# Kernel tuning notes

Measured on AMD Instinct MI355X. Metric: run time of the kernel, lower is better.

The kernel has to match this reference:

```python
import jax, jax.numpy as jnp
import numpy as np

B, H, W, C = 32, 512, 512, 3


def dct2_matrix(N):
    # Orthonormal DCT-II basis: D[k, n] = s_k * sqrt(2/N) * cos(pi*(2n+1)*k/(2N))
    n = np.arange(N)
    k = n[:, None]
    D = np.cos(np.pi * (2 * n[None, :] + 1) * k / (2.0 * N)) * np.sqrt(2.0 / N)
    D[0, :] *= 1.0 / np.sqrt(2.0)  # ortho scaling of DC row
    return jnp.asarray(D, dtype=jnp.float32)


def setup_inputs() -> dict:
    key = jax.random.key(0)
    x = jax.random.normal(key, (B, H, W, C), dtype=jnp.float32)
    return {"x": x}


def reference(x) -> jnp.ndarray:
    # 2D DCT-II (ortho) along height and width, channels untouched.
    Dh = dct2_matrix(x.shape[1])  # [H, H]
    Dw = dct2_matrix(x.shape[2])  # [W, W]
    y = jnp.einsum('kh,bhwc->bkwc', Dh, x)   # DCT over height
    y = jnp.einsum('lw,bkwc->bklc', Dw, y)   # DCT over width
    return y
```

## Files before the change

### kernel.cpp

```cpp
#include <hip/hip_runtime.h>
#include <stdint.h>


typedef __bf16 bf16_t;
typedef bf16_t bf16x8 __attribute__((ext_vector_type(8)));
typedef float  f32x4  __attribute__((ext_vector_type(4)));

__device__ __forceinline__ uint32_t f2bf(float f) {
    union { float f; uint32_t u; } v; v.f = f;
    uint32_t r = v.u + 0x7fffu + ((v.u >> 16) & 1u);
    return r >> 16;
}

__device__ __forceinline__ f32x4 mfma16(bf16x8 a, bf16x8 b, f32x4 c) {
    return __builtin_amdgcn_mfma_f32_16x16x32_bf16(a, b, c, 0, 0, 0);
}

__device__ __forceinline__ void load_lds16(const void* g, void* l) {
    __builtin_amdgcn_global_load_lds(
        (const __attribute__((address_space(1))) uint32_t*)g,
        (__attribute__((address_space(3))) uint32_t*)l, 16, 0, 0);
}

__global__ __launch_bounds__(256) void gen_dct(uint16_t* __restrict__ Dbf) {
    int idx = blockIdx.x * 256 + threadIdx.x;
    int k = idx >> 9, h = idx & 511;
    int phase = ((2 * h + 1) * k) & 2047;
    float ang = (float)phase * 3.0679615757712823e-3f;
    float s = (k == 0) ? 0.04419417382415922f : 0.0625f;
    Dbf[idx] = (uint16_t)f2bf(__cosf(ang) * s);
}

__global__ __launch_bounds__(256) void xpose(const float* __restrict__ x,
                                             uint16_t* __restrict__ Xt) {
    const int jt = blockIdx.x, hb = blockIdx.y, b = blockIdx.z;
    const int t = threadIdx.x;
    const int jl = t & 127, hh = t >> 7;
    const int jg = jt * 128 + jl;
    const int w = jg / 3, c = jg - 3 * w;
    const int wr = ((w >> 8) << 8) + ((w & 255) >> 1) + ((w & 1) << 7);
    const int jr = c * 512 + wr;
    const float* src = x + (size_t)b * 786432 +
                       (size_t)(hb * 32 + hh * 16) * 1536 + jg;
    float v[16];
#pragma unroll
    for (int r = 0; r < 16; ++r) v[r] = src[(size_t)r * 1536];
    uint32_t p[8];
#pragma unroll
    for (int i = 0; i < 8; ++i)
        p[i] = f2bf(v[2 * i]) | (f2bf(v[2 * i + 1]) << 16);
    size_t dst = ((size_t)b * 1536 + jr) * 512 + hb * 32 + hh * 16;
    *(uint4*)&Xt[dst]     = make_uint4(p[0], p[1], p[2], p[3]);
    *(uint4*)&Xt[dst + 8] = make_uint4(p[4], p[5], p[6], p[7]);
}

__global__ __launch_bounds__(512, 2) void gemm1(const uint16_t* __restrict__ Xt,
                                                const uint16_t* __restrict__ Dbf,
                                                uint16_t* __restrict__ Y) {
    __shared__ __align__(16) uint16_t Al[128 * 64];
    __shared__ __align__(16) uint16_t Bl[256 * 64];
    const int t = threadIdx.x;
    const int lane = t & 63, wv = t >> 6;
    const int wm = wv >> 2, wn = wv & 3;
    const int nt = blockIdx.x;
    const int mt = blockIdx.y;
    const int b  = blockIdx.z;

    const int qa0 = t, qa1 = t + 512;
    const int ma0 = qa0 >> 3, ga0 = (qa0 & 7) ^ (ma0 & 7);
    const int ma1 = qa1 >> 3, ga1 = (qa1 & 7) ^ (ma1 & 7);
    const uint16_t* As0 = Dbf + (size_t)(mt * 128 + ma0) * 512 + ga0 * 8;
    const uint16_t* As1 = Dbf + (size_t)(mt * 128 + ma1) * 512 + ga1 * 8;
    const uint16_t* Bs[4];
    int qb[4];
#pragma unroll
    for (int i = 0; i < 4; ++i) {
        qb[i] = t + 512 * i;
        int mb = qb[i] >> 3, gb = (qb[i] & 7) ^ (mb & 7);
        Bs[i] = Xt + ((size_t)b * 1536 + nt * 256 + mb) * 512 + gb * 8;
    }

    f32x4 acc[4][4] = {};

    for (int kt = 0; kt < 8; ++kt) {
        __syncthreads();
        load_lds16(As0 + kt * 64, Al + qa0 * 8);
        load_lds16(As1 + kt * 64, Al + qa1 * 8);
#pragma unroll
        for (int i = 0; i < 4; ++i)
            load_lds16(Bs[i] + kt * 64, Bl + qb[i] * 8);
        __syncthreads();

#pragma unroll
        for (int ks = 0; ks < 2; ++ks) {
            bf16x8 aq[4], bq[4];
#pragma unroll
            for (int mf = 0; mf < 4; ++mf) {
                int row = wm * 64 + mf * 16 + (lane & 15);
                int sl = (ks * 4 + (lane >> 4)) ^ (row & 7);
                aq[mf] = *(const bf16x8*)&Al[row * 64 + sl * 8];
            }
#pragma unroll
            for (int f = 0; f < 4; ++f) {
                int col = (wn + 4 * f) * 16 + (lane & 15);
                int sl = (ks * 4 + (lane >> 4)) ^ (col & 7);
                bq[f] = *(const bf16x8*)&Bl[col * 64 + sl * 8];
            }
#pragma unroll
            for (int mf = 0; mf < 4; ++mf)
#pragma unroll
                for (int f = 0; f < 4; ++f)
                    acc[mf][f] = mfma16(aq[mf], bq[f], acc[mf][f]);
        }
    }

    const int cch = nt >> 1, whalf = nt & 1;
#pragma unroll
    for (int mf = 0; mf < 4; ++mf)
#pragma unroll
        for (int fp = 0; fp < 2; ++fp) {
            int kbase = mt * 128 + wm * 64 + mf * 16 + ((lane >> 4) << 2);
            int u = wn + 4 * fp;
            int w = whalf * 256 + 2 * (u * 16 + (lane & 15));
#pragma unroll
            for (int r = 0; r < 4; ++r) {
                uint32_t pk = f2bf(acc[mf][fp][r]) |
                              (f2bf(acc[mf][fp + 2][r]) << 16);
                *(uint32_t*)&Y[(size_t)b * 786432 + (size_t)(kbase + r) * 1536 +
                               cch * 512 + w] = pk;
            }
        }
}

__global__ __launch_bounds__(512, 4) void gemm2(const uint16_t* __restrict__ Y,
                                                const uint16_t* __restrict__ Dbf,
                                                float* __restrict__ out) {
    __shared__ __align__(16) char smem[49408];
    uint16_t* Al = (uint16_t*)smem;
    uint16_t* Bl = (uint16_t*)(smem + 12288);
    float*    El = (float*)smem;
    const int t = threadIdx.x;
    const int lane = t & 63, wv = t >> 6;
    const int wm = wv >> 2, wn = wv & 3;
    const int mt = blockIdx.x;
    const int lt = blockIdx.y;
    const int b  = blockIdx.z;
    const size_t yb = (size_t)b * 786432;

    const int qa0 = t, qa1 = t + 512;
    const int ma0 = qa0 >> 3, ga0 = (qa0 & 7) ^ (ma0 & 7);
    const int ma1 = qa1 >> 3, ga1 = (qa1 & 7) ^ (ma1 & 7);
    const uint16_t* As0 = Y + yb + (size_t)(mt * 96 + ma0) * 512 + ga0 * 8;
    const uint16_t* As1 = Y + yb + (size_t)(mt * 96 + ma1) * 512 + ga1 * 8;
    const uint16_t* Bs[4];
    int qb[4];
#pragma unroll
    for (int i = 0; i < 4; ++i) {
        qb[i] = t + 512 * i;
        int mb = qb[i] >> 3, gb = (qb[i] & 7) ^ (mb & 7);
        Bs[i] = Dbf + (size_t)(lt * 256 + mb) * 512 + gb * 8;
    }

    f32x4 acc[3][4] = {};

    for (int kt = 0; kt < 8; ++kt) {
        __syncthreads();
        load_lds16(As0 + kt * 64, Al + qa0 * 8);
        if (t < 256) load_lds16(As1 + kt * 64, Al + qa1 * 8);
#pragma unroll
        for (int i = 0; i < 4; ++i)
            load_lds16(Bs[i] + kt * 64, Bl + qb[i] * 8);
        __syncthreads();

#pragma unroll
        for (int ks = 0; ks < 2; ++ks) {
            bf16x8 aq[3], bq[4];
#pragma unroll
            for (int mf = 0; mf < 3; ++mf) {
                int row = wm * 48 + mf * 16 + (lane & 15);
                int sl = (ks * 4 + (lane >> 4)) ^ (row & 7);
                aq[mf] = *(const bf16x8*)&Al[row * 64 + sl * 8];
            }
#pragma unroll
            for (int f = 0; f < 4; ++f) {
                int col = wn * 64 + f * 16 + (lane & 15);
                int sl = (ks * 4 + (lane >> 4)) ^ (col & 7);
                bq[f] = *(const bf16x8*)&Bl[col * 64 + sl * 8];
            }
#pragma unroll
            for (int mf = 0; mf < 3; ++mf)
#pragma unroll
                for (int f = 0; f < 4; ++f)
                    acc[mf][f] = mfma16(aq[mf], bq[f], acc[mf][f]);
        }
    }

    const int kloc = t >> 5, zrow = t & 31;
#pragma unroll
    for (int rnd = 0; rnd < 2; ++rnd) {
        __syncthreads();
        if (wm == rnd) {
#pragma unroll
            for (int mf = 0; mf < 3; ++mf)
#pragma unroll
                for (int f = 0; f < 4; ++f) {
                    int row = mf * 16 + ((lane >> 4) << 2);
                    int col = wn * 64 + f * 16 + (lane & 15);
#pragma unroll
                    for (int r = 0; r < 4; ++r)
                        El[(row + r) * 257 + col] = acc[mf][f][r];
                }
        }
        __syncthreads();
        int kbase = mt * 32 + rnd * 16;
        size_t ob = (size_t)b * 786432 + (size_t)(kbase + kloc) * 1536 + lt * 768;
#pragma unroll
        for (int q4 = 0; q4 < 6; ++q4) {
            int z0 = zrow * 24 + q4 * 4;
            float4 v;
            v.x = El[(kloc * 3 + ((z0 + 0) % 3)) * 257 + (z0 + 0) / 3];
            v.y = El[(kloc * 3 + ((z0 + 1) % 3)) * 257 + (z0 + 1) / 3];
            v.z = El[(kloc * 3 + ((z0 + 2) % 3)) * 257 + (z0 + 2) / 3];
            v.w = El[(kloc * 3 + ((z0 + 3) % 3)) * 257 + (z0 + 3) / 3];
            *(float4*)&out[ob + z0] = v;
        }
    }
}

extern "C" void kernel_launch(void* const* d_in, const int* in_sizes, int n_in,
                              void* d_out, int out_size, void* d_ws, size_t ws_size,
                              hipStream_t stream) {
    (void)in_sizes; (void)n_in; (void)out_size;
    const float* x = (const float*)d_in[0];
    float* out = (float*)d_out;
    uint16_t* Dbf = (uint16_t*)d_ws;
    uint16_t* Yw  = (uint16_t*)d_ws + 512 * 512;
    size_t need = (size_t)512 * 512 * 2 + (size_t)2 * 32 * 1536 * 512 * 2;
    uint16_t* Xt = (ws_size >= need)
                     ? (uint16_t*)d_ws + 512 * 512 + (size_t)32 * 1536 * 512
                     : (uint16_t*)d_out;

    gen_dct<<<1024, 256, 0, stream>>>(Dbf);
    dim3 gt(12, 16, 32);
    xpose<<<gt, 256, 0, stream>>>(x, Xt);
    dim3 g1(6, 4, 32);
    gemm1<<<g1, 512, 0, stream>>>(Xt, Dbf, Yw);
    dim3 g2(16, 2, 32);
    gemm2<<<g2, 512, 0, stream>>>(Yw, Dbf, out);
}
```

Before: 278.6 us.

## Widen transpose kernel work per thread and use 32-bit offsets in GEMMs

```diff
diff --git a/kernel.cpp b/kernel.cpp
--- a/kernel.cpp
+++ b/kernel.cpp
@@ -35,26 +35,30 @@
                                              uint16_t* __restrict__ Xt) {
     const int jt = blockIdx.x, hb = blockIdx.y, b = blockIdx.z;
     const int t = threadIdx.x;
-    const int jl = t & 127, hh = t >> 7;
-    const int jg = jt * 128 + jl;
+    const int jg = jt * 256 + t;
     const int w = jg / 3, c = jg - 3 * w;
     const int wr = ((w >> 8) << 8) + ((w & 255) >> 1) + ((w & 1) << 7);
     const int jr = c * 512 + wr;
-    const float* src = x + (size_t)b * 786432 +
-                       (size_t)(hb * 32 + hh * 16) * 1536 + jg;
-    float v[16];
-#pragma unroll
-    for (int r = 0; r < 16; ++r) v[r] = src[(size_t)r * 1536];
-    uint32_t p[8];
-#pragma unroll
-    for (int i = 0; i < 8; ++i)
-        p[i] = f2bf(v[2 * i]) | (f2bf(v[2 * i + 1]) << 16);
-    size_t dst = ((size_t)b * 1536 + jr) * 512 + hb * 32 + hh * 16;
-    *(uint4*)&Xt[dst]     = make_uint4(p[0], p[1], p[2], p[3]);
-    *(uint4*)&Xt[dst + 8] = make_uint4(p[4], p[5], p[6], p[7]);
-}
-
-__global__ __launch_bounds__(512, 2) void gemm1(const uint16_t* __restrict__ Xt,
+    const float* src = x + (size_t)b * 786432 + (size_t)(hb * 128) * 1536 + jg;
+    uint16_t* dst = Xt + ((size_t)b * 1536 + jr) * 512 + hb * 128;
+#pragma unroll
+    for (int hc = 0; hc < 4; ++hc) {
+        float v[32];
+#pragma unroll
+        for (int r = 0; r < 32; ++r)
+            v[r] = src[(size_t)(hc * 32 + r) * 1536];
+        uint32_t p[16];
+#pragma unroll
+        for (int i = 0; i < 16; ++i)
+            p[i] = f2bf(v[2 * i]) | (f2bf(v[2 * i + 1]) << 16);
+#pragma unroll
+        for (int u = 0; u < 4; ++u)
+            *(uint4*)&dst[hc * 32 + u * 8] =
+                make_uint4(p[4 * u], p[4 * u + 1], p[4 * u + 2], p[4 * u + 3]);
+    }
+}
+
+__global__ __launch_bounds__(512, 4) void gemm1(const uint16_t* __restrict__ Xt,
                                                 const uint16_t* __restrict__ Dbf,
                                                 uint16_t* __restrict__ Y) {
     __shared__ __align__(16) uint16_t Al[128 * 64];
@@ -69,26 +73,26 @@
     const int qa0 = t, qa1 = t + 512;
     const int ma0 = qa0 >> 3, ga0 = (qa0 & 7) ^ (ma0 & 7);
     const int ma1 = qa1 >> 3, ga1 = (qa1 & 7) ^ (ma1 & 7);
-    const uint16_t* As0 = Dbf + (size_t)(mt * 128 + ma0) * 512 + ga0 * 8;
-    const uint16_t* As1 = Dbf + (size_t)(mt * 128 + ma1) * 512 + ga1 * 8;
-    const uint16_t* Bs[4];
-    int qb[4];
+    const uint32_t aoff0 = (uint32_t)(mt * 128 + ma0) * 512 + ga0 * 8;
+    const uint32_t aoff1 = (uint32_t)(mt * 128 + ma1) * 512 + ga1 * 8;
+    uint32_t boff[4];
 #pragma unroll
     for (int i = 0; i < 4; ++i) {
-        qb[i] = t + 512 * i;
-        int mb = qb[i] >> 3, gb = (qb[i] & 7) ^ (mb & 7);
-        Bs[i] = Xt + ((size_t)b * 1536 + nt * 256 + mb) * 512 + gb * 8;
-    }
+        int q = t + 512 * i;
+        int mb = q >> 3, gb = (q & 7) ^ (mb & 7);
+        boff[i] = (uint32_t)(nt * 256 + mb) * 512 + gb * 8;
+    }
+    const uint16_t* Xb = Xt + (size_t)b * 786432;
 
     f32x4 acc[4][4] = {};
 
     for (int kt = 0; kt < 8; ++kt) {
         __syncthreads();
-        load_lds16(As0 + kt * 64, Al + qa0 * 8);
-        load_lds16(As1 + kt * 64, Al + qa1 * 8);
+        load_lds16(Dbf + aoff0 + kt * 64, Al + qa0 * 8);
+        load_lds16(Dbf + aoff1 + kt * 64, Al + qa1 * 8);
 #pragma unroll
         for (int i = 0; i < 4; ++i)
-            load_lds16(Bs[i] + kt * 64, Bl + qb[i] * 8);
+            load_lds16(Xb + boff[i] + kt * 64, Bl + (t + 512 * i) * 8);
         __syncthreads();
 
 #pragma unroll
@@ -150,26 +154,26 @@
     const int qa0 = t, qa1 = t + 512;
     const int ma0 = qa0 >> 3, ga0 = (qa0 & 7) ^ (ma0 & 7);
     const int ma1 = qa1 >> 3, ga1 = (qa1 & 7) ^ (ma1 & 7);
-    const uint16_t* As0 = Y + yb + (size_t)(mt * 96 + ma0) * 512 + ga0 * 8;
-    const uint16_t* As1 = Y + yb + (size_t)(mt * 96 + ma1) * 512 + ga1 * 8;
-    const uint16_t* Bs[4];
-    int qb[4];
+    const uint32_t aoff0 = (uint32_t)(mt * 96 + ma0) * 512 + ga0 * 8;
+    const uint32_t aoff1 = (uint32_t)(mt * 96 + ma1) * 512 + ga1 * 8;
+    uint32_t boff[4];
 #pragma unroll
     for (int i = 0; i < 4; ++i) {
-        qb[i] = t + 512 * i;
-        int mb = qb[i] >> 3, gb = (qb[i] & 7) ^ (mb & 7);
-        Bs[i] = Dbf + (size_t)(lt * 256 + mb) * 512 + gb * 8;
-    }
+        int q = t + 512 * i;
+        int mb = q >> 3, gb = (q & 7) ^ (mb & 7);
+        boff[i] = (uint32_t)(lt * 256 + mb) * 512 + gb * 8;
+    }
+    const uint16_t* Yb = Y + yb;
 
     f32x4 acc[3][4] = {};
 
     for (int kt = 0; kt < 8; ++kt) {
         __syncthreads();
-        load_lds16(As0 + kt * 64, Al + qa0 * 8);
-        if (t < 256) load_lds16(As1 + kt * 64, Al + qa1 * 8);
+        load_lds16(Yb + aoff0 + kt * 64, Al + qa0 * 8);
+        if (t < 256) load_lds16(Yb + aoff1 + kt * 64, Al + qa1 * 8);
 #pragma unroll
         for (int i = 0; i < 4; ++i)
-            load_lds16(Bs[i] + kt * 64, Bl + qb[i] * 8);
+            load_lds16(Dbf + boff[i] + kt * 64, Bl + (t + 512 * i) * 8);
         __syncthreads();
 
 #pragma unroll
@@ -241,7 +245,7 @@
                      : (uint16_t*)d_out;
 
     gen_dct<<<1024, 256, 0, stream>>>(Dbf);
-    dim3 gt(12, 16, 32);
+    dim3 gt(6, 4, 32);
     xpose<<<gt, 256, 0, stream>>>(x, Xt);
     dim3 g1(6, 4, 32);
     gemm1<<<g1, 512, 0, stream>>>(Xt, Dbf, Yw);
```

Result: slower. 285.2 us (+2.3%).
